# Optimization experiments

Measured on AMD Instinct MI355X. Metric: run time of the kernel, lower is better.

Reference implementation:

```python
import jax, jax.numpy as jnp
import numpy as np

T, B, E, H = 2048, 2, 1024, 16
DH = E // H
SCALE = DH ** -0.5
NEG = jnp.finfo(jnp.float32).min


def setup_inputs() -> dict:
    key = jax.random.key(0)
    ks = jax.random.split(key, 10)
    s = 0.02
    query = jax.random.normal(ks[0], (T, B, E), dtype=jnp.float32)
    key_padding_mask = jax.random.randint(ks[1], (B, T), 0, 2).astype(bool)
    # causal additive mask, broadcastable over (bsz, heads, tgt, src)
    causal = jnp.triu(jnp.ones((T, T), dtype=bool), k=1)
    attn_mask = jnp.where(causal, NEG, 0.0).astype(jnp.float32)[None, None]
    Wq = jax.random.normal(ks[2], (E, E), jnp.float32) * s
    bq = jax.random.normal(ks[3], (E,), jnp.float32) * s
    Wk = jax.random.normal(ks[4], (E, E), jnp.float32) * s
    bk = jax.random.normal(ks[5], (E,), jnp.float32) * s
    Wv = jax.random.normal(ks[6], (E, E), jnp.float32) * s
    bv = jax.random.normal(ks[7], (E,), jnp.float32) * s
    Wo = jax.random.normal(ks[8], (E, E), jnp.float32) * s
    bo = jax.random.normal(ks[9], (E,), jnp.float32) * s
    return {"query": query, "key_padding_mask": key_padding_mask, "attn_mask": attn_mask,
            "Wq": Wq, "bq": bq, "Wk": Wk, "bk": bk, "Wv": Wv, "bv": bv, "Wo": Wo, "bo": bo}


def _heads(x):
    # [T, B, E] -> [B, H, T, DH]
    return x.reshape(T, B, H, DH).transpose(1, 2, 0, 3)


def reference(query, key_padding_mask, attn_mask, Wq, bq, Wk, bk, Wv, bv, Wo, bo):
    # projections (torch Linear: x @ W.T + b); q scaled as in module
    q = _heads((query @ Wq.T + bq) * SCALE)          # [B,H,T,DH]
    k = _heads(query @ Wk.T + bk)                    # [B,H,S,DH] (self-attn: S=T)
    v = _heads(query @ Wv.T + bv)
    scores = jnp.einsum('bhtd,bhsd->bhts', q, k)     # [B,H,T,S]
    scores = scores + attn_mask                      # additive causal mask
    # key_padding_mask True -> masked_fill with dtype min
    scores = jnp.where(key_padding_mask[:, None, None, :], NEG, scores)
    probs = jax.nn.softmax(scores, axis=-1)
    ctx = jnp.einsum('bhts,bhsd->bhtd', probs, v)    # [B,H,T,DH]
    ctx = ctx.transpose(2, 0, 1, 3).reshape(T, B, E) # back to [T,B,E]
    return ctx @ Wo.T + bo
```

## Files before the change

### kernel.cpp

```cpp
#include <hip/hip_runtime.h>
#include <hip/hip_bf16.h>
#include <stdint.h>

typedef unsigned short u16;
typedef uint32_t u32;
typedef unsigned long long u64;
typedef __attribute__((ext_vector_type(8))) short bf16x8;
typedef __attribute__((ext_vector_type(4))) float f32x4;
typedef __attribute__((ext_vector_type(16))) float f32x16;
typedef __attribute__((ext_vector_type(4))) u32 u32x4;

#define T_SEQ 2048

__device__ __forceinline__ float bf2f(u16 u) {
  union { u32 i; float f; } v; v.i = ((u32)u) << 16; return v.f;
}
__device__ __forceinline__ u16 f2bf(float f) {
  union { float f; u32 i; } v; v.f = f;
  u32 u = v.i;
  return (u16)((u + 0x7fffu + ((u >> 16) & 1u)) >> 16);
}

#if __has_builtin(__builtin_amdgcn_exp2f)
#define EXP2F(x) __builtin_amdgcn_exp2f(x)
#else
#define EXP2F(x) exp2f(x)
#endif

__device__ __forceinline__ u32 permpack(float lo, float hi) {
#if __has_builtin(__builtin_amdgcn_perm)
  return __builtin_amdgcn_perm(__float_as_uint(hi), __float_as_uint(lo), 0x07060302u);
#else
  return (__float_as_uint(hi) & 0xFFFF0000u) | (__float_as_uint(lo) >> 16);
#endif
}

__device__ __forceinline__ void gload_lds16(const void* g, void* l) {
  __builtin_amdgcn_global_load_lds(
      (const __attribute__((address_space(1))) void*)g,
      (__attribute__((address_space(3))) void*)l, 16, 0, 0);
}

__global__ __launch_bounds__(256) void cvt_kernel(const float* __restrict__ src,
                                                  u16* __restrict__ dst, int n) {
  int i = (blockIdx.x * 256 + threadIdx.x) * 4;
  if (i + 3 < n) {
    const float4 v = *(const float4*)(src + i);
    ushort4 o;
    o.x = f2bf(v.x); o.y = f2bf(v.y); o.z = f2bf(v.z); o.w = f2bf(v.w);
    *(ushort4*)(dst + i) = o;
  }
}

__global__ __launch_bounds__(256) void cvt4_kernel(
    const float* __restrict__ s0, const float* __restrict__ s1,
    const float* __restrict__ s2, const float* __restrict__ s3,
    u16* __restrict__ dst) {
  const int z = blockIdx.y;
  const float* src = (z == 0) ? s0 : (z == 1) ? s1 : (z == 2) ? s2 : s3;
  int i = (blockIdx.x * 256 + threadIdx.x) * 4;
  const float4 v = *(const float4*)(src + i);
  ushort4 o;
  o.x = f2bf(v.x); o.y = f2bf(v.y); o.z = f2bf(v.z); o.w = f2bf(v.w);
  *(ushort4*)(dst + (size_t)z * 1048576 + i) = o;
}

__device__ __forceinline__ void gemm_core_128x64(
    f32x4 acc[2][4], const u16* __restrict__ A, const u16* __restrict__ Bw,
    int bm, int bn, u16* As, u16* Bs)
{
  const int tid = threadIdx.x;
  const int w = tid >> 6, lane = tid & 63, g = lane >> 4, c = lane & 15;
  for (int k0 = 0; k0 < 1024; k0 += 64) {
    __syncthreads();
    #pragma unroll
    for (int is = 0; is < 4; ++is) {
      int o = (is*4 + w)*1024 + lane*16;
      int row = o >> 7, c16 = (o >> 4) & 7;
      gload_lds16(A + (size_t)(bm*128 + row)*1024 + k0 + (c16 ^ (row & 7))*8,
                  (char*)As + (is*4 + w)*1024);
    }
    #pragma unroll
    for (int is = 0; is < 2; ++is) {
      int o = (is*4 + w)*1024 + lane*16;
      int row = o >> 7, c16 = (o >> 4) & 7;
      gload_lds16(Bw + (size_t)(bn*64 + row)*1024 + k0 + (c16 ^ (row & 7))*8,
                  (char*)Bs + (is*4 + w)*1024);
    }
    __syncthreads();
    bf16x8 af[2][2], bfr[4][2];
    #pragma unroll
    for (int mf = 0; mf < 2; ++mf)
      #pragma unroll
      for (int kc = 0; kc < 2; ++kc) {
        int row = w*32 + mf*16 + c;
        int colb = kc*64 + g*16;
        af[mf][kc] = *(const bf16x8*)((const char*)As + row*128 + (colb ^ ((row & 7) << 4)));
      }
    #pragma unroll
    for (int nf = 0; nf < 4; ++nf)
      #pragma unroll
      for (int kc = 0; kc < 2; ++kc) {
        int row = nf*16 + c;
        int colb = kc*64 + g*16;
        bfr[nf][kc] = *(const bf16x8*)((const char*)Bs + row*128 + (colb ^ ((row & 7) << 4)));
      }
    #pragma unroll
    for (int mf = 0; mf < 2; ++mf)
      #pragma unroll
      for (int nf = 0; nf < 4; ++nf)
        #pragma unroll
        for (int kc = 0; kc < 2; ++kc)
          acc[mf][nf] = __builtin_amdgcn_mfma_f32_16x16x32_bf16(
              af[mf][kc], bfr[nf][kc], acc[mf][nf], 0, 0, 0);
  }
}

__global__ __launch_bounds__(256, 2) void gemm_qkv(
    const u16* __restrict__ Abf, const u16* __restrict__ Wbf,
    const float* __restrict__ bq, const float* __restrict__ bk,
    const float* __restrict__ bv, u16* __restrict__ qkvh)
{
  __shared__ __align__(16) u16 As[128*64];
  __shared__ __align__(16) u16 Bs[64*64];
  f32x4 acc[2][4];
  #pragma unroll
  for (int mf = 0; mf < 2; ++mf)
    #pragma unroll
    for (int nf = 0; nf < 4; ++nf) acc[mf][nf] = (f32x4){0.f,0.f,0.f,0.f};
  const int z = blockIdx.z;
  gemm_core_128x64(acc, Abf, Wbf + (size_t)z*1048576, blockIdx.x, blockIdx.y, As, Bs);
  const float* bias = (z == 0) ? bq : (z == 1) ? bk : bv;
  const float scl = (z == 0) ? 0.18033688011112043f : 1.0f;
  u16* dst = qkvh + (size_t)z * 4194304;
  const int tid = threadIdx.x, w = tid >> 6, lane = tid & 63, g = lane >> 4, c = lane & 15;
  #pragma unroll
  for (int mf = 0; mf < 2; ++mf)
    #pragma unroll
    for (int nf = 0; nf < 4; ++nf) {
      int col = blockIdx.y*64 + nf*16 + c;
      float bcol = bias[col];
      int h = col >> 6, d = col & 63;
      #pragma unroll
      for (int r = 0; r < 4; ++r) {
        int row = blockIdx.x*128 + w*32 + mf*16 + g*4 + r;
        int t = row >> 1, bb = row & 1;
        float v = (acc[mf][nf][r] + bcol) * scl;
        dst[(size_t)(bb*16 + h)*131072 + (size_t)t*64 + d] = f2bf(v);
      }
    }
}

__global__ __launch_bounds__(256, 2) void gemm_out(
    const u16* __restrict__ ctx2, const u16* __restrict__ Wobf,
    const float* __restrict__ bo, float* __restrict__ out)
{
  __shared__ __align__(16) u16 As[128*64];
  __shared__ __align__(16) u16 Bs[64*64];
  f32x4 acc[2][4];
  #pragma unroll
  for (int mf = 0; mf < 2; ++mf)
    #pragma unroll
    for (int nf = 0; nf < 4; ++nf) acc[mf][nf] = (f32x4){0.f,0.f,0.f,0.f};
  gemm_core_128x64(acc, ctx2, Wobf, blockIdx.x, blockIdx.y, As, Bs);
  const int tid = threadIdx.x, w = tid >> 6, lane = tid & 63, g = lane >> 4, c = lane & 15;
  #pragma unroll
  for (int mf = 0; mf < 2; ++mf)
    #pragma unroll
    for (int nf = 0; nf < 4; ++nf) {
      int col = blockIdx.y*64 + nf*16 + c;
      float bcol = bo[col];
      #pragma unroll
      for (int r = 0; r < 4; ++r) {
        int row = blockIdx.x*128 + w*32 + mf*16 + g*4 + r;
        out[(size_t)row*1024 + col] = acc[mf][nf][r] + bcol;
      }
    }
}

__global__ __launch_bounds__(256) void vtrans_kernel(const u16* __restrict__ Vh,
                                                     u16* __restrict__ Vt,
                                                     float* __restrict__ vs) {
  __shared__ u16 tile[64][72];
  const int bh = blockIdx.x >> 5, tc = blockIdx.x & 31;
  const int t0 = tc * 64;
  const int tid = threadIdx.x;
  {
    const int tl = tid >> 2, d0 = (tid & 3) * 16;
    const u16* src = Vh + (size_t)bh*131072 + (size_t)(t0 + tl)*64 + d0;
    bf16x8 a = *(const bf16x8*)src;
    bf16x8 b2 = *(const bf16x8*)(src + 8);
    #pragma unroll
    for (int j = 0; j < 8; ++j) {
      tile[d0 + j][tl] = (u16)a[j];
      tile[d0 + 8 + j][tl] = (u16)b2[j];
    }
  }
  __syncthreads();
  {
    const int d = tid >> 2, tq = (tid & 3) * 16;
    bf16x8 o0, o1;
    float s = 0.f;
    #pragma unroll
    for (int j = 0; j < 8; ++j) {
      u16 x0 = tile[d][tq + j], x1 = tile[d][tq + 8 + j];
      o0[j] = (short)x0; o1[j] = (short)x1;
      s += bf2f(x0) + bf2f(x1);
    }
    u16* dst = Vt + (size_t)bh*131072 + (size_t)d*2048 + t0 + tq;
    *(bf16x8*)dst = o0;
    *(bf16x8*)(dst + 8) = o1;
    s += __shfl_xor(s, 1, 64);
    s += __shfl_xor(s, 2, 64);
    if ((tid & 3) == 0) atomicAdd(&vs[bh*64 + d], s);
  }
}

#define ZERO16 (f32x16){0.f,0.f,0.f,0.f,0.f,0.f,0.f,0.f,0.f,0.f,0.f,0.f,0.f,0.f,0.f,0.f}
#define NEGINF (-__builtin_inff())

__global__ __launch_bounds__(64, 2) void flash_attn(
    const u16* __restrict__ Qh, const u16* __restrict__ Kh,
    const u16* __restrict__ Vt, const int* __restrict__ kpm,
    const float* __restrict__ vsum, u16* __restrict__ ctx2,
    u16* __restrict__ pctx, float* __restrict__ pml)
{
  const int lane = threadIdx.x;
  const int l31 = lane & 31, hi = lane >> 5;

  const int id = blockIdx.x;
  const int xcd = id & 7, rest = id >> 3;
  const int bh = xcd * 4 + (rest & 3);
  const int pp = rest >> 2;
  int qt, ch, NS;
  if (pp < 32) { qt = pp; ch = 0; NS = 1; }
  else { int uu = pp - 32; qt = 32 + (uu >> 1); ch = uu & 1; NS = 2; }
  const int b = bh >> 4, h = bh & 15;
  const int q0 = qt * 32;
  const size_t hbase = (size_t)bh * 131072;
  const int nt = (qt >> 1) + 1;
  int lo, hicap;
  if (NS == 1) { lo = 0; hicap = nt; }
  else { int h1 = nt >> 1; lo = ch ? h1 : 0; hicap = ch ? nt : h1; }
  const int q = q0 + l31;

  bf16x8 qfrag[4];
  #pragma unroll
  for (int kt = 0; kt < 4; ++kt)
    qfrag[kt] = *(const bf16x8*)(Qh + hbase + (size_t)q*64 + kt*16 + hi*8);

  bf16x8 kreg[2][4];
  #pragma unroll
  for (int sub = 0; sub < 2; ++sub)
    #pragma unroll
    for (int kt = 0; kt < 4; ++kt)
      kreg[sub][kt] = *(const bf16x8*)(Kh + hbase + (size_t)(lo*64 + sub*32 + l31)*64 + kt*16 + hi*8);

  int kpmv_cur = kpm[b*T_SEQ + lo*64 + lane];
  int kpmv_nxt = 0;

  float mrow = NEGINF, lrow = 0.f;
  f32x16 cacc0 = ZERO16, cacc1 = ZERO16;

  for (int t = lo; t < hicap; ++t) {
    const int s0 = t * 64;
    const bool notLast = (t + 1 < hicap);
    const bool diag = (t == nt - 1);

    bf16x8 vf[2][4];
    #pragma unroll
    for (int db = 0; db < 2; ++db)
      #pragma unroll
      for (int ks = 0; ks < 4; ++ks)
        vf[db][ks] = *(const bf16x8*)(Vt + hbase + (size_t)(db*32 + l31)*2048 + s0 + ks*16 + hi*8);

    f32x16 st0 = ZERO16, st1 = ZERO16;
    __builtin_amdgcn_s_setprio(1);
    #pragma unroll
    for (int kt = 0; kt < 4; ++kt) {
      st0 = __builtin_amdgcn_mfma_f32_32x32x16_bf16(kreg[0][kt], qfrag[kt], st0, 0, 0, 0);
      st1 = __builtin_amdgcn_mfma_f32_32x32x16_bf16(kreg[1][kt], qfrag[kt], st1, 0, 0, 0);
    }
    __builtin_amdgcn_s_setprio(0);

    if (notLast) {
      #pragma unroll
      for (int sub = 0; sub < 2; ++sub)
        #pragma unroll
        for (int kt = 0; kt < 4; ++kt)
          kreg[sub][kt] = *(const bf16x8*)(Kh + hbase + (size_t)(s0 + 64 + sub*32 + l31)*64 + kt*16 + hi*8);
      kpmv_nxt = kpm[b*T_SEQ + s0 + 64 + lane];
    }

    {
      const u64 mask = __ballot(kpmv_cur != 0);
      const u32 m0 = (u32)mask, m1 = (u32)(mask >> 32);
      const u64 m4 = mask >> 4;
      const u32 m4l = (u32)m4, m4h = (u32)(m4 >> 32);
      const u32 w0 = hi ? m4l : m0;
      const u32 w1 = hi ? m4h : m1;
      const int lim = q - s0 - 4*hi;
      #pragma unroll
      for (int m = 0; m < 4; ++m) {
        u32 nib0 = (w0 >> (m*8)) & 15u;
        u32 nib1 = (w1 >> (m*8)) & 15u;
        if (diag) {
          int t0c = lim - m*8;       int c0 = min(max(t0c + 1, 0), 4);
          int t1c = lim - 32 - m*8;  int c1 = min(max(t1c + 1, 0), 4);
          nib0 |= (0xFu << c0) & 0xFu;
          nib1 |= (0xFu << c1) & 0xFu;
        }
        #pragma unroll
        for (int r = 0; r < 4; ++r) {
          if ((nib0 >> r) & 1) st0[m*4 + r] = NEGINF;
          if ((nib1 >> r) & 1) st1[m*4 + r] = NEGINF;
        }
      }
      float t8[8];
      #pragma unroll
      for (int i = 0; i < 8; ++i)
        t8[i] = fmaxf(fmaxf(st0[i], st0[i+8]), fmaxf(st1[i], st1[i+8]));
      float t4a = fmaxf(t8[0], t8[4]), t4b = fmaxf(t8[1], t8[5]);
      float t4c = fmaxf(t8[2], t8[6]), t4d = fmaxf(t8[3], t8[7]);
      float rm = fmaxf(fmaxf(t4a, t4b), fmaxf(t4c, t4d));
      rm = fmaxf(rm, __shfl_xor(rm, 32, 64));
      const float mn = fmaxf(mrow, rm);
      const bool dead = (mn == NEGINF);
      const float sc = dead ? 1.f : EXP2F(mrow - mn);
      mrow = mn;
      float ps = 0.f;
      #pragma unroll
      for (int i = 0; i < 16; ++i) {
        float pv = dead ? 0.f : EXP2F(st0[i] - mn);
        st0[i] = pv; ps += pv;
      }
      #pragma unroll
      for (int i = 0; i < 16; ++i) {
        float pv = dead ? 0.f : EXP2F(st1[i] - mn);
        st1[i] = pv; ps += pv;
      }
      ps += __shfl_xor(ps, 32, 64);
      lrow = lrow * sc + ps;
      #pragma unroll
      for (int i = 0; i < 16; ++i) { cacc0[i] *= sc; cacc1[i] *= sc; }
    }

    u32 pk[8][2];
    #pragma unroll
    for (int m = 0; m < 4; ++m) {
      pk[m][0]   = permpack(st0[m*4+0], st0[m*4+1]);
      pk[m][1]   = permpack(st0[m*4+2], st0[m*4+3]);
      pk[4+m][0] = permpack(st1[m*4+0], st1[m*4+1]);
      pk[4+m][1] = permpack(st1[m*4+2], st1[m*4+3]);
    }
    bf16x8 pf[4];
    #pragma unroll
    for (int ks = 0; ks < 4; ++ks) {
      u32 own0 = pk[2*ks][0],   own1 = pk[2*ks][1];
      u32 oth0 = pk[2*ks+1][0], oth1 = pk[2*ks+1][1];
      u32 r0 = __shfl_xor(hi ? own0 : oth0, 32, 64);
      u32 r1 = __shfl_xor(hi ? own1 : oth1, 32, 64);
      u32 w0 = hi ? r0 : own0;
      u32 w1 = hi ? r1 : own1;
      u32 w2 = hi ? oth0 : r0;
      u32 w3 = hi ? oth1 : r1;
      u32x4 wv = {w0, w1, w2, w3};
      pf[ks] = __builtin_bit_cast(bf16x8, wv);
    }

    __builtin_amdgcn_s_setprio(1);
    #pragma unroll
    for (int ks = 0; ks < 4; ++ks)
      cacc0 = __builtin_amdgcn_mfma_f32_32x32x16_bf16(vf[0][ks], pf[ks], cacc0, 0, 0, 0);
    #pragma unroll
    for (int ks = 0; ks < 4; ++ks)
      cacc1 = __builtin_amdgcn_mfma_f32_32x32x16_bf16(vf[1][ks], pf[ks], cacc1, 0, 0, 0);
    __builtin_amdgcn_s_setprio(0);

    kpmv_cur = kpmv_nxt;
  }

  if (NS == 1) {
    const bool dead = (lrow == 0.f);
    const float rl = dead ? 0.f : 1.f / lrow;
    #pragma unroll
    for (int subd = 0; subd < 2; ++subd) {
      #pragma unroll
      for (int m = 0; m < 4; ++m) {
        const int d0 = subd*32 + hi*4 + m*8;
        float v0 = (subd ? cacc1[m*4+0] : cacc0[m*4+0]) * rl;
        float v1 = (subd ? cacc1[m*4+1] : cacc0[m*4+1]) * rl;
        float v2 = (subd ? cacc1[m*4+2] : cacc0[m*4+2]) * rl;
        float v3 = (subd ? cacc1[m*4+3] : cacc0[m*4+3]) * rl;
        if (dead) {
          const float* vs = vsum + bh*64 + d0;
          v0 = vs[0] * (1.0f/2048.0f);
          v1 = vs[1] * (1.0f/2048.0f);
          v2 = vs[2] * (1.0f/2048.0f);
          v3 = vs[3] * (1.0f/2048.0f);
        }
        ushort4 o;
        o.x = f2bf(v0); o.y = f2bf(v1); o.z = f2bf(v2); o.w = f2bf(v3);
        *(ushort4*)(ctx2 + (size_t)(q*2 + b)*1024 + h*64 + d0) = o;
      }
    }
  } else {
    const int slot = ((bh << 5) + (qt - 32))*2 + ch;
    u16* pc = pctx + (size_t)slot*2048 + (size_t)l31*64;
    #pragma unroll
    for (int subd = 0; subd < 2; ++subd) {
      #pragma unroll
      for (int m = 0; m < 4; ++m) {
        const int d0 = subd*32 + hi*4 + m*8;
        const f32x16& cc = subd ? cacc1 : cacc0;
        ushort4 o;
        o.x = f2bf(cc[m*4+0]); o.y = f2bf(cc[m*4+1]);
        o.z = f2bf(cc[m*4+2]); o.w = f2bf(cc[m*4+3]);
        *(ushort4*)(pc + d0) = o;
      }
    }
    if (!hi) {
      float2 ml; ml.x = mrow; ml.y = lrow;
      *(float2*)(pml + (size_t)slot*64 + l31*2) = ml;
    }
  }
}

__global__ __launch_bounds__(64) void combine_kernel(
    const u16* __restrict__ pctx, const float* __restrict__ pml,
    const float* __restrict__ vsum, u16* __restrict__ ctx2)
{
  const int qtm = blockIdx.x, bh = blockIdx.y;
  const int qt = 32 + qtm;
  const int b = bh >> 4, h = bh & 15;
  const int lane = threadIdx.x;
  const int qr = lane >> 1, d0 = (lane & 1) * 32;
  const int slot0 = ((bh << 5) + qtm)*2;
  const float* ml0 = pml + (size_t)slot0*64 + qr*2;
  const float* ml1 = pml + (size_t)(slot0+1)*64 + qr*2;
  const float m1 = ml0[0], l1 = ml0[1];
  const float m2 = ml1[0], l2 = ml1[1];
  const float ms = fmaxf(m1, m2);
  bool dead = (ms == NEGINF);
  const float w1 = dead ? 0.f : EXP2F(m1 - ms);
  const float w2 = dead ? 0.f : EXP2F(m2 - ms);
  const float lt = w1*l1 + w2*l2;
  dead = dead || (lt == 0.f);
  const float rl = dead ? 0.f : 1.f / lt;
  const u16* c1 = pctx + ((size_t)slot0*32 + qr)*64 + d0;
  const u16* c2 = pctx + ((size_t)(slot0+1)*32 + qr)*64 + d0;
  const int qrow = qt*32 + qr;
  u16* dst = ctx2 + (size_t)(qrow*2 + b)*1024 + h*64 + d0;
  #pragma unroll
  for (int g2 = 0; g2 < 4; ++g2) {
    bf16x8 a = *(const bf16x8*)(c1 + g2*8);
    bf16x8 bb = *(const bf16x8*)(c2 + g2*8);
    bf16x8 o;
    #pragma unroll
    for (int j = 0; j < 8; ++j) {
      float v = (w1*bf2f((u16)a[j]) + w2*bf2f((u16)bb[j])) * rl;
      if (dead) v = vsum[bh*64 + d0 + g2*8 + j] * (1.0f/2048.0f);
      o[j] = (short)f2bf(v);
    }
    *(bf16x8*)(dst + g2*8) = o;
  }
}

extern "C" void kernel_launch(void* const* d_in, const int* in_sizes, int n_in,
                              void* d_out, int out_size, void* d_ws, size_t ws_size,
                              hipStream_t stream) {
  const float* query = (const float*)d_in[0];
  const int*   kpm   = (const int*)d_in[1];
  const float* Wq = (const float*)d_in[3];
  const float* bq = (const float*)d_in[4];
  const float* Wk = (const float*)d_in[5];
  const float* bk = (const float*)d_in[6];
  const float* Wv = (const float*)d_in[7];
  const float* bv = (const float*)d_in[8];
  const float* Wo = (const float*)d_in[9];
  const float* bo = (const float*)d_in[10];

  char* ws = (char*)d_ws;
  u16*   qbf  = (u16*)(ws);
  u16*   Vt   = (u16*)(ws);
  u16*   wbf  = (u16*)(ws + 8388608);
  u16*   qkvh = (u16*)(ws + 16777216);
  u16*   pctx = (u16*)(ws + 33554432);
  u16*   ctx2 = (u16*)(ws + 41943040);
  float* vsum = (float*)(ws + 50331648);
  float* pml  = (float*)(ws + 50339840);

  cvt_kernel<<<dim3(4096), 256, 0, stream>>>(query, qbf, 4194304);
  cvt4_kernel<<<dim3(1024, 4), 256, 0, stream>>>(Wq, Wk, Wv, Wo, wbf);

  hipMemsetAsync(vsum, 0, 2048 * sizeof(float), stream);

  gemm_qkv<<<dim3(32, 16, 3), 256, 0, stream>>>(qbf, wbf, bq, bk, bv, qkvh);
  vtrans_kernel<<<dim3(1024), 256, 0, stream>>>(qkvh + 2*4194304, Vt, vsum);
  flash_attn<<<dim3(3072), 64, 0, stream>>>(qkvh, qkvh + 1*4194304,
                                            Vt, kpm, vsum, ctx2, pctx, pml);
  combine_kernel<<<dim3(32, 32), 64, 0, stream>>>(pctx, pml, vsum, ctx2);
  gemm_out<<<dim3(32, 16), 256, 0, stream>>>(ctx2, wbf + 3*1048576, bo, (float*)d_out);
}
```

Baseline: 153.1 us.

## Widen GEMM tiles to 128x128 with 8 waves and add lazy softmax rescaling

The QKV and output GEMMs now use 128x128 block tiles with 512 threads (8 waves laid out 4x2), halving the grid and cutting redundant A-tile loads from global memory. In flash attention, the running max and the accumulator rescale are now updated only when some lane's block max exceeds the stored max by more than 8 (in log2 units). The exp accumulation is also split into four partial sums for more ILP. Lazy rescaling lets exponentials reach up to 2^8 before normalisation, a small fp32 range risk, and the larger GEMM blocks may lower occupancy or leave fewer blocks to spread across CUs.

```diff
diff --git a/kernel.cpp b/kernel.cpp
--- a/kernel.cpp
+++ b/kernel.cpp
@@ -65,27 +65,28 @@
   *(ushort4*)(dst + (size_t)z * 1048576 + i) = o;
 }
 
-__device__ __forceinline__ void gemm_core_128x64(
+__device__ __forceinline__ void gemm_core_128x128(
     f32x4 acc[2][4], const u16* __restrict__ A, const u16* __restrict__ Bw,
     int bm, int bn, u16* As, u16* Bs)
 {
   const int tid = threadIdx.x;
   const int w = tid >> 6, lane = tid & 63, g = lane >> 4, c = lane & 15;
+  const int wr = (w & 3) * 32, wc = (w >> 2) * 64;
   for (int k0 = 0; k0 < 1024; k0 += 64) {
     __syncthreads();
     #pragma unroll
-    for (int is = 0; is < 4; ++is) {
-      int o = (is*4 + w)*1024 + lane*16;
+    for (int is = 0; is < 2; ++is) {
+      int o = (is*8 + w)*1024 + lane*16;
       int row = o >> 7, c16 = (o >> 4) & 7;
       gload_lds16(A + (size_t)(bm*128 + row)*1024 + k0 + (c16 ^ (row & 7))*8,
-                  (char*)As + (is*4 + w)*1024);
+                  (char*)As + (is*8 + w)*1024);
     }
     #pragma unroll
     for (int is = 0; is < 2; ++is) {
-      int o = (is*4 + w)*1024 + lane*16;
+      int o = (is*8 + w)*1024 + lane*16;
       int row = o >> 7, c16 = (o >> 4) & 7;
-      gload_lds16(Bw + (size_t)(bn*64 + row)*1024 + k0 + (c16 ^ (row & 7))*8,
-                  (char*)Bs + (is*4 + w)*1024);
+      gload_lds16(Bw + (size_t)(bn*128 + row)*1024 + k0 + (c16 ^ (row & 7))*8,
+                  (char*)Bs + (is*8 + w)*1024);
     }
     __syncthreads();
     bf16x8 af[2][2], bfr[4][2];
@@ -93,7 +94,7 @@
     for (int mf = 0; mf < 2; ++mf)
       #pragma unroll
       for (int kc = 0; kc < 2; ++kc) {
-        int row = w*32 + mf*16 + c;
+        int row = wr + mf*16 + c;
         int colb = kc*64 + g*16;
         af[mf][kc] = *(const bf16x8*)((const char*)As + row*128 + (colb ^ ((row & 7) << 4)));
       }
@@ -101,7 +102,7 @@
     for (int nf = 0; nf < 4; ++nf)
       #pragma unroll
       for (int kc = 0; kc < 2; ++kc) {
-        int row = nf*16 + c;
+        int row = wc + nf*16 + c;
         int colb = kc*64 + g*16;
         bfr[nf][kc] = *(const bf16x8*)((const char*)Bs + row*128 + (colb ^ ((row & 7) << 4)));
       }
@@ -116,34 +117,35 @@
   }
 }
 
-__global__ __launch_bounds__(256, 2) void gemm_qkv(
+__global__ __launch_bounds__(512, 2) void gemm_qkv(
     const u16* __restrict__ Abf, const u16* __restrict__ Wbf,
     const float* __restrict__ bq, const float* __restrict__ bk,
     const float* __restrict__ bv, u16* __restrict__ qkvh)
 {
   __shared__ __align__(16) u16 As[128*64];
-  __shared__ __align__(16) u16 Bs[64*64];
+  __shared__ __align__(16) u16 Bs[128*64];
   f32x4 acc[2][4];
   #pragma unroll
   for (int mf = 0; mf < 2; ++mf)
     #pragma unroll
     for (int nf = 0; nf < 4; ++nf) acc[mf][nf] = (f32x4){0.f,0.f,0.f,0.f};
   const int z = blockIdx.z;
-  gemm_core_128x64(acc, Abf, Wbf + (size_t)z*1048576, blockIdx.x, blockIdx.y, As, Bs);
+  gemm_core_128x128(acc, Abf, Wbf + (size_t)z*1048576, blockIdx.x, blockIdx.y, As, Bs);
   const float* bias = (z == 0) ? bq : (z == 1) ? bk : bv;
   const float scl = (z == 0) ? 0.18033688011112043f : 1.0f;
   u16* dst = qkvh + (size_t)z * 4194304;
   const int tid = threadIdx.x, w = tid >> 6, lane = tid & 63, g = lane >> 4, c = lane & 15;
+  const int wr = (w & 3) * 32, wc = (w >> 2) * 64;
   #pragma unroll
   for (int mf = 0; mf < 2; ++mf)
     #pragma unroll
     for (int nf = 0; nf < 4; ++nf) {
-      int col = blockIdx.y*64 + nf*16 + c;
+      int col = blockIdx.y*128 + wc + nf*16 + c;
       float bcol = bias[col];
       int h = col >> 6, d = col & 63;
       #pragma unroll
       for (int r = 0; r < 4; ++r) {
-        int row = blockIdx.x*128 + w*32 + mf*16 + g*4 + r;
+        int row = blockIdx.x*128 + wr + mf*16 + g*4 + r;
         int t = row >> 1, bb = row & 1;
         float v = (acc[mf][nf][r] + bcol) * scl;
         dst[(size_t)(bb*16 + h)*131072 + (size_t)t*64 + d] = f2bf(v);
@@ -151,28 +153,29 @@
     }
 }
 
-__global__ __launch_bounds__(256, 2) void gemm_out(
+__global__ __launch_bounds__(512, 2) void gemm_out(
     const u16* __restrict__ ctx2, const u16* __restrict__ Wobf,
     const float* __restrict__ bo, float* __restrict__ out)
 {
   __shared__ __align__(16) u16 As[128*64];
-  __shared__ __align__(16) u16 Bs[64*64];
+  __shared__ __align__(16) u16 Bs[128*64];
   f32x4 acc[2][4];
   #pragma unroll
   for (int mf = 0; mf < 2; ++mf)
     #pragma unroll
     for (int nf = 0; nf < 4; ++nf) acc[mf][nf] = (f32x4){0.f,0.f,0.f,0.f};
-  gemm_core_128x64(acc, ctx2, Wobf, blockIdx.x, blockIdx.y, As, Bs);
+  gemm_core_128x128(acc, ctx2, Wobf, blockIdx.x, blockIdx.y, As, Bs);
   const int tid = threadIdx.x, w = tid >> 6, lane = tid & 63, g = lane >> 4, c = lane & 15;
+  const int wr = (w & 3) * 32, wc = (w >> 2) * 64;
   #pragma unroll
   for (int mf = 0; mf < 2; ++mf)
     #pragma unroll
     for (int nf = 0; nf < 4; ++nf) {
-      int col = blockIdx.y*64 + nf*16 + c;
+      int col = blockIdx.y*128 + wc + nf*16 + c;
       float bcol = bo[col];
       #pragma unroll
       for (int r = 0; r < 4; ++r) {
-        int row = blockIdx.x*128 + w*32 + mf*16 + g*4 + r;
+        int row = blockIdx.x*128 + wr + mf*16 + g*4 + r;
         out[(size_t)row*1024 + col] = acc[mf][nf][r] + bcol;
       }
     }
@@ -324,25 +327,35 @@
       float t4c = fmaxf(t8[2], t8[6]), t4d = fmaxf(t8[3], t8[7]);
       float rm = fmaxf(fmaxf(t4a, t4b), fmaxf(t4c, t4d));
       rm = fmaxf(rm, __shfl_xor(rm, 32, 64));
-      const float mn = fmaxf(mrow, rm);
-      const bool dead = (mn == NEGINF);
-      const float sc = dead ? 1.f : EXP2F(mrow - mn);
-      mrow = mn;
-      float ps = 0.f;
-      #pragma unroll
-      for (int i = 0; i < 16; ++i) {
-        float pv = dead ? 0.f : EXP2F(st0[i] - mn);
-        st0[i] = pv; ps += pv;
-      }
-      #pragma unroll
-      for (int i = 0; i < 16; ++i) {
-        float pv = dead ? 0.f : EXP2F(st1[i] - mn);
-        st1[i] = pv; ps += pv;
-      }
+
+      const bool need = (rm > mrow + 8.f) || (mrow < -1e30f);
+      if (__any(need)) {
+        const float mn = fmaxf(mrow, rm);
+        const float sc = (mn < -1e30f) ? 1.f : EXP2F(mrow - mn);
+        mrow = mn;
+        lrow *= sc;
+        #pragma unroll
+        for (int i = 0; i < 16; ++i) { cacc0[i] *= sc; cacc1[i] *= sc; }
+      }
+      const bool dead = (mrow < -1e30f);
+      float a0 = 0.f, a1 = 0.f, a2 = 0.f, a3 = 0.f;
+      #pragma unroll
+      for (int i = 0; i < 16; i += 4) {
+        float p0 = dead ? 0.f : EXP2F(st0[i+0] - mrow); st0[i+0] = p0; a0 += p0;
+        float p1 = dead ? 0.f : EXP2F(st0[i+1] - mrow); st0[i+1] = p1; a1 += p1;
+        float p2 = dead ? 0.f : EXP2F(st0[i+2] - mrow); st0[i+2] = p2; a2 += p2;
+        float p3 = dead ? 0.f : EXP2F(st0[i+3] - mrow); st0[i+3] = p3; a3 += p3;
+      }
+      #pragma unroll
+      for (int i = 0; i < 16; i += 4) {
+        float p0 = dead ? 0.f : EXP2F(st1[i+0] - mrow); st1[i+0] = p0; a0 += p0;
+        float p1 = dead ? 0.f : EXP2F(st1[i+1] - mrow); st1[i+1] = p1; a1 += p1;
+        float p2 = dead ? 0.f : EXP2F(st1[i+2] - mrow); st1[i+2] = p2; a2 += p2;
+        float p3 = dead ? 0.f : EXP2F(st1[i+3] - mrow); st1[i+3] = p3; a3 += p3;
+      }
+      float ps = (a0 + a1) + (a2 + a3);
       ps += __shfl_xor(ps, 32, 64);
-      lrow = lrow * sc + ps;
-      #pragma unroll
-      for (int i = 0; i < 16; ++i) { cacc0[i] *= sc; cacc1[i] *= sc; }
+      lrow += ps;
     }
 
     u32 pk[8][2];
@@ -495,10 +508,10 @@
 
   hipMemsetAsync(vsum, 0, 2048 * sizeof(float), stream);
 
-  gemm_qkv<<<dim3(32, 16, 3), 256, 0, stream>>>(qbf, wbf, bq, bk, bv, qkvh);
+  gemm_qkv<<<dim3(32, 8, 3), 512, 0, stream>>>(qbf, wbf, bq, bk, bv, qkvh);
   vtrans_kernel<<<dim3(1024), 256, 0, stream>>>(qkvh + 2*4194304, Vt, vsum);
   flash_attn<<<dim3(3072), 64, 0, stream>>>(qkvh, qkvh + 1*4194304,
                                             Vt, kpm, vsum, ctx2, pctx, pml);
   combine_kernel<<<dim3(32, 32), 64, 0, stream>>>(pctx, pml, vsum, ctx2);
-  gemm_out<<<dim3(32, 16), 256, 0, stream>>>(ctx2, wbf + 3*1048576, bo, (float*)d_out);
-}
+  gemm_out<<<dim3(32, 8), 512, 0, stream>>>(ctx2, wbf + 3*1048576, bo, (float*)d_out);
+}
```

Result: no change. 152.2 us (-0.5%).
